# Optimization experiments

Measured on AMD Instinct MI355X. Metric: run time of the kernel, lower is better.

Reference implementation:

```python
import jax, jax.numpy as jnp
import numpy as np

N_HEAD = 16

def setup_inputs() -> dict:
    key = jax.random.key(0)
    k1, k2, k3 = jax.random.split(key, 3)
    B, S, D = 4, 2048, 1024
    x = jax.random.normal(k1, (B, S, D), dtype=jnp.float32)
    w_attn = jax.random.normal(k2, (D, 3 * D), dtype=jnp.float32) * 0.02
    b_attn = jnp.zeros((3 * D,), dtype=jnp.float32)
    w_proj = jax.random.normal(k3, (D, D), dtype=jnp.float32) * 0.02
    b_proj = jnp.zeros((D,), dtype=jnp.float32)
    return {"x": x, "w_attn": w_attn, "b_attn": b_attn, "w_proj": w_proj, "b_proj": b_proj}

def reference(x, w_attn, b_attn, w_proj, b_proj):
    B, S, D = x.shape
    H = N_HEAD
    dh = D // H
    # c_attn (fan_in_fan_out Conv1D-style: y = x @ W + b)
    qkv = x @ w_attn + b_attn                      # [B,S,3D]
    q, k, v = jnp.split(qkv, 3, axis=-1)
    q = q.reshape(B, S, H, dh).transpose(0, 2, 1, 3)   # [B,H,S,dh]
    k = k.reshape(B, S, H, dh).transpose(0, 2, 3, 1)   # [B,H,dh,S]  (split_heads k=True)
    v = v.reshape(B, S, H, dh).transpose(0, 2, 1, 3)   # [B,H,S,dh]
    # scores = Q K^T, scaled by sqrt(d_head) since scale=True
    w = jnp.einsum('bhid,bhdj->bhij', q, k) / jnp.sqrt(jnp.asarray(dh, x.dtype))
    # causal mask blending exactly as original: w*b - 1e10*(1-b)
    b = jnp.tril(jnp.ones((S, S), dtype=x.dtype))[None, None]
    w = w * b - 1e10 * (1.0 - b)
    w = jax.nn.softmax(w, axis=-1)
    a = jnp.einsum('bhij,bhjd->bhid', w, v)        # [B,H,S,dh]
    a = a.transpose(0, 2, 1, 3).reshape(B, S, D)   # merge_heads
    out = a @ w_proj + b_proj                      # c_proj
    present = jnp.stack((k.transpose(0, 1, 3, 2), v))  # [2,B,H,S,dh]
    return out, present
```

## Files before the change

### kernel.cpp

```cpp
#include <hip/hip_runtime.h>
#include <stdint.h>

typedef unsigned short u16;
typedef __attribute__((ext_vector_type(8))) __bf16 bf16x8;
typedef __attribute__((ext_vector_type(4))) __bf16 bf16x4v;
typedef __attribute__((ext_vector_type(4))) float f32x4;
typedef __attribute__((ext_vector_type(4))) unsigned short u16x4;
typedef __attribute__((ext_vector_type(8))) unsigned short u16x8;

#define MFMA16(a,b,c) __builtin_amdgcn_mfma_f32_16x16x32_bf16(a,b,c,0,0,0)

static __device__ __forceinline__ float fexp2(float x){
#if __has_builtin(__builtin_amdgcn_exp2f)
  return __builtin_amdgcn_exp2f(x);
#else
  float r; asm("v_exp_f32 %0, %1" : "=v"(r) : "v"(x)); return r;
#endif
}

static __device__ __forceinline__ u16 f2b(float f){
  uint32_t u = __float_as_uint(f);
  u += 0x7fffu + ((u >> 16) & 1u);
  return (u16)(u >> 16);
}

static __device__ __forceinline__ void gload_lds16(const void* g, void* l){
  __builtin_amdgcn_global_load_lds(
      (__attribute__((address_space(1))) void*)(uintptr_t)g,
      (__attribute__((address_space(3))) void*)(uintptr_t)l,
      16, 0, 0);
}

__global__ __launch_bounds__(256) void cvt_bf16(const float* __restrict__ in,
                                                u16* __restrict__ out, int n){
  int i = (blockIdx.x * 256 + threadIdx.x) * 4;
  if (i >= n) return;
  float4 v = *(const float4*)(in + i);
  u16x4 o;
  o.x = f2b(v.x); o.y = f2b(v.y); o.z = f2b(v.z); o.w = f2b(v.w);
  *(u16x4*)(out + i) = o;
}

__global__ __launch_bounds__(256) void transpose_cvt(const float* __restrict__ in,
                                                     u16* __restrict__ out,
                                                     int K, int N){
  __shared__ float tile[32][33];
  const int nb = blockIdx.x * 32, kb = blockIdx.y * 32;
  const int tx = threadIdx.x, ty = threadIdx.y;
#pragma unroll
  for (int i = 0; i < 32; i += 8)
    tile[ty + i][tx] = in[(size_t)(kb + ty + i) * N + nb + tx];
  __syncthreads();
#pragma unroll
  for (int i = 0; i < 32; i += 8)
    out[(size_t)(nb + ty + i) * K + kb + tx] = f2b(tile[tx][ty + i]);
}

template<int MODE>
__global__ __launch_bounds__(512, 2) void gemm_pipe(
    const u16* __restrict__ A, const u16* __restrict__ Bt,
    const float* __restrict__ bias, float* __restrict__ Cout,
    u16* __restrict__ q_bf, u16* __restrict__ k_bf, u16* __restrict__ vT_bf,
    int N, int K)
{
  extern __shared__ u16 smem[];
  const int nT = K >> 5;
  const int tid = threadIdx.x;
  const int w = tid >> 6, lane = tid & 63;
  const int l15 = lane & 15, lhi = lane >> 4;
  const int wr = w >> 1, wc = w & 1;
  const int mBase = blockIdx.y * 256, nBase = blockIdx.x * 128;

  const int r0 = tid >> 2;
  const int ch = (tid & 3) ^ ((r0 >> 1) & 3);
  const u16* Ag  = A  + (size_t)(mBase + r0) * K + ch * 8;
  const u16* Ag2 = Ag + (size_t)128 * K;
  const u16* Bg  = Bt + (size_t)(nBase + r0) * K + ch * 8;

  f32x4 acc[4][4];
#pragma unroll
  for (int i = 0; i < 4; ++i)
#pragma unroll
    for (int j = 0; j < 4; ++j) acc[i][j] = f32x4{0.f, 0.f, 0.f, 0.f};

  auto stage = [&](int kt){
    char* buf = (char*)smem + (kt % 3) * 24576;
    const int kb = kt << 5;
    gload_lds16(Ag  + kb, buf + tid * 16);
    gload_lds16(Ag2 + kb, buf + 8192 + tid * 16);
    gload_lds16(Bg  + kb, buf + 16384 + tid * 16);
  };

  stage(0); stage(1);

  for (int kt = 0; kt < nT; ++kt){
    if (kt == nT - 1) asm volatile("s_waitcnt vmcnt(0)" ::: "memory");
    else              asm volatile("s_waitcnt vmcnt(3)" ::: "memory");
    __builtin_amdgcn_s_barrier();
    const char* Ab = (const char*)smem + (kt % 3) * 24576;
    const char* Bb = Ab + 16384;
#define LDT(base, row) (*(const bf16x8*)((base) + ((row) << 6) + ((lhi ^ (((row) >> 1) & 3)) << 4)))
    bf16x8 a0, a1, a2, a3, b0, b1, b2, b3;
    {
      const int ar = wr * 64 + l15;
      a0 = LDT(Ab, ar); a1 = LDT(Ab, ar + 16); a2 = LDT(Ab, ar + 32); a3 = LDT(Ab, ar + 48);
      const int br = wc * 64 + l15;
      b0 = LDT(Bb, br); b1 = LDT(Bb, br + 16); b2 = LDT(Bb, br + 32); b3 = LDT(Bb, br + 48);
    }
#undef LDT
    if (kt + 2 < nT) stage(kt + 2);
    __builtin_amdgcn_s_setprio(1);
    acc[0][0] = MFMA16(a0, b0, acc[0][0]); acc[0][1] = MFMA16(a0, b1, acc[0][1]);
    acc[0][2] = MFMA16(a0, b2, acc[0][2]); acc[0][3] = MFMA16(a0, b3, acc[0][3]);
    acc[1][0] = MFMA16(a1, b0, acc[1][0]); acc[1][1] = MFMA16(a1, b1, acc[1][1]);
    acc[1][2] = MFMA16(a1, b2, acc[1][2]); acc[1][3] = MFMA16(a1, b3, acc[1][3]);
    acc[2][0] = MFMA16(a2, b0, acc[2][0]); acc[2][1] = MFMA16(a2, b1, acc[2][1]);
    acc[2][2] = MFMA16(a2, b2, acc[2][2]); acc[2][3] = MFMA16(a2, b3, acc[2][3]);
    acc[3][0] = MFMA16(a3, b0, acc[3][0]); acc[3][1] = MFMA16(a3, b1, acc[3][1]);
    acc[3][2] = MFMA16(a3, b2, acc[3][2]); acc[3][3] = MFMA16(a3, b3, acc[3][3]);
    __builtin_amdgcn_s_setprio(0);
  }

  if (MODE == 0){
#pragma unroll
    for (int ni = 0; ni < 4; ++ni){
      const int col = nBase + wc * 64 + ni * 16 + l15;
      const float bv = bias[col];
#pragma unroll
      for (int mi = 0; mi < 4; ++mi)
#pragma unroll
        for (int r = 0; r < 4; ++r){
          const int row = mBase + wr * 64 + mi * 16 + lhi * 4 + r;
          Cout[(size_t)row * N + col] = acc[mi][ni][r] + bv;
        }
    }
    return;
  }

  const int sec = nBase >> 10;
  const int nn0 = nBase & 1023;
  const int bb_ = mBase >> 11;
  const int s0  = mBase & 2047;

  if (sec == 2){
#pragma unroll
    for (int ni = 0; ni < 4; ++ni){
      const int c = wc * 64 + ni * 16 + l15;
      const int nn = nn0 + c;
      const int h = nn >> 6, d = nn & 63;
      const float bv = bias[nBase + c];
#pragma unroll
      for (int mi = 0; mi < 4; ++mi){
        const int sb = s0 + wr * 64 + mi * 16 + lhi * 4;
        u16x4 pk;
#pragma unroll
        for (int r = 0; r < 4; ++r){
          const float v = acc[mi][ni][r] + bv;
          pk[r] = f2b(v);
          Cout[16777216 + ((size_t)(bb_ * 16 + h) * 2048 + sb + r) * 64 + d] = v;
        }
        *(u16x4*)(vT_bf + ((size_t)(bb_ * 16 + h) * 64 + d) * 2048 + sb) = pk;
      }
    }
    return;
  }

  __syncthreads();
  const float qscl = (sec == 0) ? 0.1803368801111204f : 1.0f;
#pragma unroll
  for (int ni = 0; ni < 4; ++ni){
    const int c = wc * 64 + ni * 16 + l15;
    const float bv = bias[nBase + c];
#pragma unroll
    for (int mi = 0; mi < 4; ++mi)
#pragma unroll
      for (int r = 0; r < 4; ++r){
        const int rl = wr * 64 + mi * 16 + lhi * 4 + r;
        smem[rl * 128 + (c ^ ((rl & 7) << 3))] = f2b((acc[mi][ni][r] + bv) * qscl);
      }
  }
  if (sec == 1){
#pragma unroll
    for (int ni = 0; ni < 4; ++ni){
      const int c = wc * 64 + ni * 16 + l15;
      const int nn = nn0 + c;
      const int h = nn >> 6, d = nn & 63;
      const float bv = bias[nBase + c];
#pragma unroll
      for (int mi = 0; mi < 4; ++mi)
#pragma unroll
        for (int r = 0; r < 4; ++r){
          const int s = s0 + wr * 64 + mi * 16 + lhi * 4 + r;
          Cout[8388608 + ((size_t)(bb_ * 16 + h) * 2048 + s) * 64 + d] = acc[mi][ni][r] + bv;
        }
    }
  }
  __syncthreads();
  {
    const int row = tid >> 1, half = tid & 1;
    u16* base = (sec == 0 ? q_bf : k_bf);
#pragma unroll
    for (int i = 0; i < 8; ++i){
      const int c0 = half * 64 + i * 8;
      const int h = (nn0 >> 6) + (c0 >> 6);
      u16x8 vv = *(const u16x8*)&smem[row * 128 + (c0 ^ ((row & 7) << 3))];
      *(u16x8*)(base + ((size_t)(bb_ * 16 + h) * 2048 + s0 + row) * 64 + (c0 & 63)) = vv;
    }
  }
}

__global__ __launch_bounds__(256) void attn_kern(
    const u16* __restrict__ q_bf, const u16* __restrict__ k_bf,
    const u16* __restrict__ vT_bf, u16* __restrict__ a_bf)
{
  const int S = 2048;
  const int id = (int)blockIdx.x + 32 * (int)blockIdx.y;
  const int xcd = id & 7, j = id >> 3;
  const int bh = xcd + 8 * (j & 7);
  const int qt = 31 - (j >> 3);

  const int tid = threadIdx.x, w = tid >> 6, lane = tid & 63;
  const int l15 = lane & 15, lhi = lane >> 4;
  const u16* qp = q_bf + (size_t)bh * S * 64;
  const char* kbytes = (const char*)(k_bf + (size_t)bh * S * 64);
  const char* vbytes = (const char*)(vT_bf + (size_t)bh * 64 * S);
  const int b = bh >> 4, h = bh & 15;

  __shared__ u16 Kbuf[2][64 * 64];
  __shared__ u16 Vbuf[2][64 * 64];
  __shared__ u16 P_all[4][16 * 64];
  char* Pc = (char*)&P_all[w][0];
  const int swz = (l15 & 7) << 4;

  const int srow = tid >> 3;
  const int sch  = (tid & 7) ^ (srow & 7);

  const int qr0 = qt * 64 + w * 16;
  const int nStage = qt + 1;

  bf16x8 qf0 = *(const bf16x8*)&qp[(qr0 + l15) * 64 + lhi * 8];
  bf16x8 qf1 = *(const bf16x8*)&qp[(qr0 + l15) * 64 + 32 + lhi * 8];

  f32x4 o[4];
#pragma unroll
  for (int df = 0; df < 4; ++df) o[df] = f32x4{0.f,0.f,0.f,0.f};
  float lsum = 0.f;

  int cur = 0;
  gload_lds16(kbytes + (size_t)srow * 128 + sch * 16,        (char*)Kbuf[0] + w * 1024);
  gload_lds16(kbytes + (size_t)(srow + 32) * 128 + sch * 16, (char*)Kbuf[0] + 4096 + w * 1024);
  gload_lds16(vbytes + (size_t)srow * 4096 + sch * 16,        (char*)Vbuf[0] + w * 1024);
  gload_lds16(vbytes + (size_t)(srow + 32) * 4096 + sch * 16, (char*)Vbuf[0] + 4096 + w * 1024);
  __syncthreads();

  for (int it = 0; it < nStage; ++it){
    const int jb = it * 64;
    if (it + 1 < nStage){
      const char* kb2 = kbytes + (size_t)(jb + 64) * 128;
      const char* vb2 = vbytes + (size_t)(jb + 64) * 2;
      char* kd = (char*)Kbuf[cur ^ 1];
      char* vd = (char*)Vbuf[cur ^ 1];
      gload_lds16(kb2 + (size_t)srow * 128 + sch * 16,        kd + w * 1024);
      gload_lds16(kb2 + (size_t)(srow + 32) * 128 + sch * 16, kd + 4096 + w * 1024);
      gload_lds16(vb2 + (size_t)srow * 4096 + sch * 16,        vd + w * 1024);
      gload_lds16(vb2 + (size_t)(srow + 32) * 4096 + sch * 16, vd + 4096 + w * 1024);
    }
    {
      const char* Kc = (const char*)Kbuf[cur];
      const char* Vc = (const char*)Vbuf[cur];
      f32x4 s[4];
      __builtin_amdgcn_s_setprio(1);
#pragma unroll
      for (int nf = 0; nf < 4; ++nf){
        const bf16x8 kf0 = *(const bf16x8*)(Kc + (((nf * 16 + l15) * 128 + 0 * 64 + lhi * 16) ^ swz));
        const bf16x8 kf1 = *(const bf16x8*)(Kc + (((nf * 16 + l15) * 128 + 1 * 64 + lhi * 16) ^ swz));
        f32x4 z = {0.f, 0.f, 0.f, 0.f};
        z = MFMA16(kf0, qf0, z);
        z = MFMA16(kf1, qf1, z);
        s[nf] = z;
      }
      __builtin_amdgcn_s_setprio(0);
      bf16x8 vf[8];
#pragma unroll
      for (int kk = 0; kk < 2; ++kk)
#pragma unroll
        for (int df = 0; df < 4; ++df)
          vf[kk*4+df] = *(const bf16x8*)(Vc + (((df * 16 + l15) * 128 + kk * 64 + lhi * 16) ^ swz));
      if (it == nStage - 1){
        const int q = qr0 + l15;
#pragma unroll
        for (int nf = 0; nf < 4; ++nf)
#pragma unroll
          for (int r = 0; r < 4; ++r){
            const int kv = jb + nf * 16 + lhi * 4 + r;
            if (kv > q) s[nf][r] = -1e10f;
          }
      }
      float p[16];
#pragma unroll
      for (int nf = 0; nf < 4; ++nf)
#pragma unroll
        for (int r = 0; r < 4; ++r) p[nf*4+r] = fexp2(s[nf][r]);
      lsum += (((p[0]+p[1])+(p[2]+p[3])) + ((p[4]+p[5])+(p[6]+p[7])))
            + (((p[8]+p[9])+(p[10]+p[11])) + ((p[12]+p[13])+(p[14]+p[15])));
#pragma unroll
      for (int nf = 0; nf < 4; ++nf){
        bf16x4v pk;
#pragma unroll
        for (int r = 0; r < 4; ++r) pk[r] = (__bf16)p[nf*4+r];
        *(bf16x4v*)(Pc + ((l15 * 128 + nf * 32 + lhi * 8) ^ swz)) = pk;
      }
      __builtin_amdgcn_s_setprio(1);
#pragma unroll
      for (int kk = 0; kk < 2; ++kk){
        const bf16x8 pa = *(const bf16x8*)(Pc + ((l15 * 128 + kk * 64 + lhi * 16) ^ swz));
#pragma unroll
        for (int df = 0; df < 4; ++df)
          o[df] = MFMA16(pa, vf[kk*4+df], o[df]);
      }
      __builtin_amdgcn_s_setprio(0);
    }
    __syncthreads();
    cur ^= 1;
  }

  {
    float rs = lsum;
    rs += __shfl_xor(rs, 16);
    rs += __shfl_xor(rs, 32);
    const float linv = 1.0f / rs;
    float lr[4];
#pragma unroll
    for (int r = 0; r < 4; ++r)
      lr[r] = __shfl(linv, (lane & 48) | (lhi * 4 + r));
#pragma unroll
    for (int r = 0; r < 4; ++r){
      const int qrow = qr0 + lhi * 4 + r;
#pragma unroll
      for (int df = 0; df < 4; ++df)
        a_bf[((size_t)b * 2048 + qrow) * 1024 + h * 64 + df * 16 + l15] = f2b(o[df][r] * lr[r]);
    }
  }
}

extern "C" void kernel_launch(void* const* d_in, const int* in_sizes, int n_in,
                              void* d_out, int out_size, void* d_ws, size_t ws_size,
                              hipStream_t stream)
{
  const float* x      = (const float*)d_in[0];
  const float* w_attn = (const float*)d_in[1];
  const float* b_attn = (const float*)d_in[2];
  const float* w_proj = (const float*)d_in[3];
  const float* b_proj = (const float*)d_in[4];
  float* out = (float*)d_out;
  char* ws = (char*)d_ws;
  const size_t MB = 1u << 20;
  u16* x_bf  = (u16*)(ws + 0);
  u16* wA_T  = (u16*)(ws + 16 * MB);
  u16* wP_T  = (u16*)(ws + 22 * MB);
  u16* q_bf  = (u16*)(ws + 24 * MB);
  u16* k_bf  = (u16*)(ws + 40 * MB);
  u16* vT_bf = (u16*)(ws + 56 * MB);
  u16* a_bf  = x_bf;

  cvt_bf16<<<dim3(8192), dim3(256), 0, stream>>>(x, x_bf, 4 * 2048 * 1024);
  transpose_cvt<<<dim3(96, 32), dim3(32, 8), 0, stream>>>(w_attn, wA_T, 1024, 3072);
  transpose_cvt<<<dim3(32, 32), dim3(32, 8), 0, stream>>>(w_proj, wP_T, 1024, 1024);
  gemm_pipe<1><<<dim3(24, 32), dim3(512), 73728, stream>>>(
      x_bf, wA_T, b_attn, out, q_bf, k_bf, vT_bf, 3072, 1024);
  attn_kern<<<dim3(32, 64), dim3(256), 0, stream>>>(q_bf, k_bf, vT_bf, a_bf);
  gemm_pipe<0><<<dim3(8, 32), dim3(512), 73728, stream>>>(
      a_bf, wP_T, b_proj, out, nullptr, nullptr, nullptr, 1024, 1024);
}
```

Measured before the change: 176.9 us.

## Double attention query tile to 128 rows per block with two 16-row fragments per wave

Each attention block now covers 128 query rows instead of 64. Every wave processes two 16-row query fragments, so each K/V tile staged in shared memory is reused twice and the grid is halved. Waves whose causal range ends earlier skip compute on the last stage but still take part in loads and barriers. The cost is higher register pressure and possible load imbalance across waves within a block.

```diff
diff --git a/kernel.cpp b/kernel.cpp
--- a/kernel.cpp
+++ b/kernel.cpp
@@ -214,10 +214,10 @@
     const u16* __restrict__ vT_bf, u16* __restrict__ a_bf)
 {
   const int S = 2048;
-  const int id = (int)blockIdx.x + 32 * (int)blockIdx.y;
+  const int id = (int)blockIdx.x + 16 * (int)blockIdx.y;
   const int xcd = id & 7, j = id >> 3;
   const int bh = xcd + 8 * (j & 7);
-  const int qt = 31 - (j >> 3);
+  const int qt = 15 - (j >> 3);
 
   const int tid = threadIdx.x, w = tid >> 6, lane = tid & 63;
   const int l15 = lane & 15, lhi = lane >> 4;
@@ -235,16 +235,19 @@
   const int srow = tid >> 3;
   const int sch  = (tid & 7) ^ (srow & 7);
 
-  const int qr0 = qt * 64 + w * 16;
-  const int nStage = qt + 1;
-
-  bf16x8 qf0 = *(const bf16x8*)&qp[(qr0 + l15) * 64 + lhi * 8];
-  bf16x8 qf1 = *(const bf16x8*)&qp[(qr0 + l15) * 64 + 32 + lhi * 8];
-
-  f32x4 o[4];
-#pragma unroll
-  for (int df = 0; df < 4; ++df) o[df] = f32x4{0.f,0.f,0.f,0.f};
-  float lsum = 0.f;
+  const int qr0 = qt * 128 + w * 32;
+  const int nStage = 2 * qt + 2;
+  const int nC = 2 * qt + 1 + (w >> 1);
+
+  bf16x8 qfA0 = *(const bf16x8*)&qp[(qr0 + l15) * 64 + lhi * 8];
+  bf16x8 qfA1 = *(const bf16x8*)&qp[(qr0 + l15) * 64 + 32 + lhi * 8];
+  bf16x8 qfB0 = *(const bf16x8*)&qp[(qr0 + 16 + l15) * 64 + lhi * 8];
+  bf16x8 qfB1 = *(const bf16x8*)&qp[(qr0 + 16 + l15) * 64 + 32 + lhi * 8];
+
+  f32x4 oA[4], oB[4];
+#pragma unroll
+  for (int df = 0; df < 4; ++df){ oA[df] = f32x4{0.f,0.f,0.f,0.f}; oB[df] = f32x4{0.f,0.f,0.f,0.f}; }
+  float lsumA = 0.f, lsumB = 0.f;
 
   int cur = 0;
   gload_lds16(kbytes + (size_t)srow * 128 + sch * 16,        (char*)Kbuf[0] + w * 1024);
@@ -265,19 +268,23 @@
       gload_lds16(vb2 + (size_t)srow * 4096 + sch * 16,        vd + w * 1024);
       gload_lds16(vb2 + (size_t)(srow + 32) * 4096 + sch * 16, vd + 4096 + w * 1024);
     }
-    {
+    if (it < nC){
       const char* Kc = (const char*)Kbuf[cur];
       const char* Vc = (const char*)Vbuf[cur];
-      f32x4 s[4];
+      f32x4 sA[4], sB[4];
       __builtin_amdgcn_s_setprio(1);
 #pragma unroll
       for (int nf = 0; nf < 4; ++nf){
         const bf16x8 kf0 = *(const bf16x8*)(Kc + (((nf * 16 + l15) * 128 + 0 * 64 + lhi * 16) ^ swz));
         const bf16x8 kf1 = *(const bf16x8*)(Kc + (((nf * 16 + l15) * 128 + 1 * 64 + lhi * 16) ^ swz));
-        f32x4 z = {0.f, 0.f, 0.f, 0.f};
-        z = MFMA16(kf0, qf0, z);
-        z = MFMA16(kf1, qf1, z);
-        s[nf] = z;
+        f32x4 zA = {0.f, 0.f, 0.f, 0.f};
+        zA = MFMA16(kf0, qfA0, zA);
+        zA = MFMA16(kf1, qfA1, zA);
+        sA[nf] = zA;
+        f32x4 zB = {0.f, 0.f, 0.f, 0.f};
+        zB = MFMA16(kf0, qfB0, zB);
+        zB = MFMA16(kf1, qfB1, zB);
+        sB[nf] = zB;
       }
       __builtin_amdgcn_s_setprio(0);
       bf16x8 vf[8];
@@ -286,59 +293,92 @@
 #pragma unroll
         for (int df = 0; df < 4; ++df)
           vf[kk*4+df] = *(const bf16x8*)(Vc + (((df * 16 + l15) * 128 + kk * 64 + lhi * 16) ^ swz));
-      if (it == nStage - 1){
-        const int q = qr0 + l15;
+      if (it == nC - 1){
+        const int qA = qr0 + l15, qB = qr0 + 16 + l15;
 #pragma unroll
         for (int nf = 0; nf < 4; ++nf)
 #pragma unroll
           for (int r = 0; r < 4; ++r){
             const int kv = jb + nf * 16 + lhi * 4 + r;
-            if (kv > q) s[nf][r] = -1e10f;
+            if (kv > qA) sA[nf][r] = -1e10f;
+            if (kv > qB) sB[nf][r] = -1e10f;
           }
       }
-      float p[16];
-#pragma unroll
-      for (int nf = 0; nf < 4; ++nf)
-#pragma unroll
-        for (int r = 0; r < 4; ++r) p[nf*4+r] = fexp2(s[nf][r]);
-      lsum += (((p[0]+p[1])+(p[2]+p[3])) + ((p[4]+p[5])+(p[6]+p[7])))
-            + (((p[8]+p[9])+(p[10]+p[11])) + ((p[12]+p[13])+(p[14]+p[15])));
-#pragma unroll
-      for (int nf = 0; nf < 4; ++nf){
-        bf16x4v pk;
-#pragma unroll
-        for (int r = 0; r < 4; ++r) pk[r] = (__bf16)p[nf*4+r];
-        *(bf16x4v*)(Pc + ((l15 * 128 + nf * 32 + lhi * 8) ^ swz)) = pk;
-      }
-      __builtin_amdgcn_s_setprio(1);
-#pragma unroll
-      for (int kk = 0; kk < 2; ++kk){
-        const bf16x8 pa = *(const bf16x8*)(Pc + ((l15 * 128 + kk * 64 + lhi * 16) ^ swz));
-#pragma unroll
-        for (int df = 0; df < 4; ++df)
-          o[df] = MFMA16(pa, vf[kk*4+df], o[df]);
-      }
-      __builtin_amdgcn_s_setprio(0);
+      {
+        float p[16];
+#pragma unroll
+        for (int nf = 0; nf < 4; ++nf)
+#pragma unroll
+          for (int r = 0; r < 4; ++r) p[nf*4+r] = fexp2(sA[nf][r]);
+        lsumA += (((p[0]+p[1])+(p[2]+p[3])) + ((p[4]+p[5])+(p[6]+p[7])))
+               + (((p[8]+p[9])+(p[10]+p[11])) + ((p[12]+p[13])+(p[14]+p[15])));
+#pragma unroll
+        for (int nf = 0; nf < 4; ++nf){
+          bf16x4v pk;
+#pragma unroll
+          for (int r = 0; r < 4; ++r) pk[r] = (__bf16)p[nf*4+r];
+          *(bf16x4v*)(Pc + ((l15 * 128 + nf * 32 + lhi * 8) ^ swz)) = pk;
+        }
+        __builtin_amdgcn_s_setprio(1);
+#pragma unroll
+        for (int kk = 0; kk < 2; ++kk){
+          const bf16x8 pa = *(const bf16x8*)(Pc + ((l15 * 128 + kk * 64 + lhi * 16) ^ swz));
+#pragma unroll
+          for (int df = 0; df < 4; ++df)
+            oA[df] = MFMA16(pa, vf[kk*4+df], oA[df]);
+        }
+        __builtin_amdgcn_s_setprio(0);
+      }
+      {
+        float p[16];
+#pragma unroll
+        for (int nf = 0; nf < 4; ++nf)
+#pragma unroll
+          for (int r = 0; r < 4; ++r) p[nf*4+r] = fexp2(sB[nf][r]);
+        lsumB += (((p[0]+p[1])+(p[2]+p[3])) + ((p[4]+p[5])+(p[6]+p[7])))
+               + (((p[8]+p[9])+(p[10]+p[11])) + ((p[12]+p[13])+(p[14]+p[15])));
+#pragma unroll
+        for (int nf = 0; nf < 4; ++nf){
+          bf16x4v pk;
+#pragma unroll
+          for (int r = 0; r < 4; ++r) pk[r] = (__bf16)p[nf*4+r];
+          *(bf16x4v*)(Pc + ((l15 * 128 + nf * 32 + lhi * 8) ^ swz)) = pk;
+        }
+        __builtin_amdgcn_s_setprio(1);
+#pragma unroll
+        for (int kk = 0; kk < 2; ++kk){
+          const bf16x8 pa = *(const bf16x8*)(Pc + ((l15 * 128 + kk * 64 + lhi * 16) ^ swz));
+#pragma unroll
+          for (int df = 0; df < 4; ++df)
+            oB[df] = MFMA16(pa, vf[kk*4+df], oB[df]);
+        }
+        __builtin_amdgcn_s_setprio(0);
+      }
     }
     __syncthreads();
     cur ^= 1;
   }
 
   {
-    float rs = lsum;
-    rs += __shfl_xor(rs, 16);
-    rs += __shfl_xor(rs, 32);
-    const float linv = 1.0f / rs;
-    float lr[4];
-#pragma unroll
-    for (int r = 0; r < 4; ++r)
-      lr[r] = __shfl(linv, (lane & 48) | (lhi * 4 + r));
+    float rsA = lsumA, rsB = lsumB;
+    rsA += __shfl_xor(rsA, 16); rsA += __shfl_xor(rsA, 32);
+    rsB += __shfl_xor(rsB, 16); rsB += __shfl_xor(rsB, 32);
+    const float invA = 1.0f / rsA, invB = 1.0f / rsB;
+    float lrA[4], lrB[4];
 #pragma unroll
     for (int r = 0; r < 4; ++r){
-      const int qrow = qr0 + lhi * 4 + r;
-#pragma unroll
-      for (int df = 0; df < 4; ++df)
-        a_bf[((size_t)b * 2048 + qrow) * 1024 + h * 64 + df * 16 + l15] = f2b(o[df][r] * lr[r]);
+      lrA[r] = __shfl(invA, (lane & 48) | (lhi * 4 + r));
+      lrB[r] = __shfl(invB, (lane & 48) | (lhi * 4 + r));
+    }
+#pragma unroll
+    for (int r = 0; r < 4; ++r){
+      const int qrowA = qr0 + lhi * 4 + r;
+      const int qrowB = qr0 + 16 + lhi * 4 + r;
+#pragma unroll
+      for (int df = 0; df < 4; ++df){
+        a_bf[((size_t)b * 2048 + qrowA) * 1024 + h * 64 + df * 16 + l15] = f2b(oA[df][r] * lrA[r]);
+        a_bf[((size_t)b * 2048 + qrowB) * 1024 + h * 64 + df * 16 + l15] = f2b(oB[df][r] * lrB[r]);
+      }
     }
   }
 }
@@ -368,7 +408,7 @@
   transpose_cvt<<<dim3(32, 32), dim3(32, 8), 0, stream>>>(w_proj, wP_T, 1024, 1024);
   gemm_pipe<1><<<dim3(24, 32), dim3(512), 73728, stream>>>(
       x_bf, wA_T, b_attn, out, q_bf, k_bf, vT_bf, 3072, 1024);
-  attn_kern<<<dim3(32, 64), dim3(256), 0, stream>>>(q_bf, k_bf, vT_bf, a_bf);
+  attn_kern<<<dim3(16, 64), dim3(256), 0, stream>>>(q_bf, k_bf, vT_bf, a_bf);
   gemm_pipe<0><<<dim3(8, 32), dim3(512), 73728, stream>>>(
       a_bf, wP_T, b_proj, out, nullptr, nullptr, nullptr, 1024, 1024);
 }
```

New measurement: 180.4 us. No clear change (+2.0%).
